# Kernel optimization log

Hardware: AMD Instinct MI355X
Metric: run time of the kernel (lower is better)

## Reference

```python
import jax, jax.numpy as jnp
import numpy as np
from jax import lax

B, C, H, W = 64, 3, 256, 256
E, D = 64, 32          # expert_nums, embed_dim
TOP_K = 2
NOISE_EPS = 0.01
ALPHA = 0.8


def setup_inputs() -> dict:
    key = jax.random.key(0)
    ks = jax.random.split(key, 16)
    n = lambda k, shape, s=0.05: jax.random.normal(k, shape, jnp.float32) * s
    return {
        "task_id": jax.random.randint(ks[0], (B,), 0, 10),
        "degradation_info": jax.random.normal(ks[1], (B, C, H, W), jnp.float32),
        "noise": jax.random.normal(ks[2], (B, E), jnp.float32),
        "mlp_w1": n(ks[3], (1, D)), "mlp_b1": jnp.zeros((D,), jnp.float32),
        "mlp_w2": n(ks[4], (D, D)), "mlp_b2": jnp.zeros((D,), jnp.float32),
        "conv1_w": n(ks[5], (16, C, 3, 3)), "conv1_b": jnp.zeros((16,), jnp.float32),
        "conv2_w": n(ks[6], (32, 16, 3, 3)), "conv2_b": jnp.zeros((32,), jnp.float32),
        "deg_w": n(ks[7], (32, D)), "deg_b": jnp.zeros((D,), jnp.float32),
        "expert_keys": jax.random.normal(ks[8], (E, D), jnp.float32),
        "gate_w": n(ks[9], (E, E)), "gate_b": jnp.zeros((E,), jnp.float32),
        "noise_w": n(ks[10], (E, E)), "noise_b": jnp.zeros((E,), jnp.float32),
    }


def _conv(x, w):
    return lax.conv_general_dilated(
        x, w, window_strides=(1, 1), padding="SAME",
        dimension_numbers=("NCHW", "OIHW", "NCHW"))


def reference(task_id, degradation_info, noise,
              mlp_w1, mlp_b1, mlp_w2, mlp_b2,
              conv1_w, conv1_b, conv2_w, conv2_b,
              deg_w, deg_b, expert_keys,
              gate_w, gate_b, noise_w, noise_b):
    # task embedding: Linear(1,D) -> ReLU -> Linear(D,D)
    t = task_id.astype(jnp.float32)[:, None]                       # [B,1]
    task_embed = jax.nn.relu(t @ mlp_w1 + mlp_b1) @ mlp_w2 + mlp_b2  # [B,D]

    # degradation conv embed: conv->relu->conv->relu->global avg pool
    h = jax.nn.relu(_conv(degradation_info, conv1_w) + conv1_b[None, :, None, None])
    h = jax.nn.relu(_conv(h, conv2_w) + conv2_b[None, :, None, None])
    feat = h.mean(axis=(2, 3))                                     # [B,32]
    deg_embed = feat @ deg_w + deg_b                               # [B,D]

    combined = task_embed + (1.0 - ALPHA) * deg_embed              # [B,D]
    sim = combined @ expert_keys.T / jnp.sqrt(jnp.float32(D))      # [B,E]
    expert_weight = jax.nn.softmax(sim, axis=1)

    clean_logits = expert_weight @ gate_w + gate_b                 # [B,E]
    stddev = jax.nn.softplus(expert_weight @ noise_w + noise_b) + NOISE_EPS
    logits = clean_logits + noise * stddev                         # train=True path

    top_logits, top_idx = lax.top_k(logits, min(TOP_K + 1, E))
    tk_logits = top_logits[:, :TOP_K]                              # [B,k]
    tk_idx = top_idx[:, :TOP_K]
    tk_gates = jax.nn.softmax(tk_logits, axis=1)

    rows = jnp.arange(logits.shape[0])[:, None]
    gates = jnp.zeros_like(logits).at[rows, tk_idx].set(tk_gates)  # scatter
    load = gates.sum(axis=0)                                       # [E]
    return gates, load
```

## Files before the change

### kernel.cpp

```cpp
#include <hip/hip_runtime.h>
#include <math.h>

typedef __attribute__((ext_vector_type(8)))  short  short8;
typedef __attribute__((ext_vector_type(4)))  short  svec4;
typedef __attribute__((ext_vector_type(4)))  float  floatx4;
typedef __attribute__((ext_vector_type(16))) float  floatx16;
typedef __attribute__((ext_vector_type(2)))  float  floatx2;
typedef __attribute__((ext_vector_type(2)))  unsigned uintx2;

__device__ __forceinline__ short bf16rne(float f) {
    unsigned u = __float_as_uint(f);
    unsigned r = (u + 0x7FFFu + ((u >> 16) & 1u)) >> 16;
    return (short)r;
}
__device__ __forceinline__ unsigned pk2(float a, float b) {
#if __has_builtin(__builtin_amdgcn_cvt_pk_bf16_f32)
    auto t = __builtin_amdgcn_cvt_pk_bf16_f32(a, b);
    unsigned u; __builtin_memcpy(&u, &t, 4); return u;
#else
    return (unsigned)(unsigned short)bf16rne(a) |
           ((unsigned)(unsigned short)bf16rne(b) << 16);
#endif
}
__device__ __forceinline__ floatx2 pkmax0(floatx2 a) {
#if __has_builtin(__builtin_elementwise_max)
    floatx2 z = {0.f, 0.f};
    return __builtin_elementwise_max(a, z);
#else
    floatx2 r; r.x = fmaxf(a.x, 0.f); r.y = fmaxf(a.y, 0.f); return r;
#endif
}

#define WS_FRAG_OFF  8192
#define WS_BIAS1_OFF (WS_FRAG_OFF + 11 * 64 * 16)
#define WS_BIAS2_OFF (WS_BIAS1_OFF + 64 * 16)

#define PLANE_B 18496

__global__ __launch_bounds__(256) void build_frags_kernel(
    const float* __restrict__ w1,
    const float* __restrict__ b1,
    const float* __restrict__ w2,
    const float* __restrict__ b2,
    void* __restrict__ ws,
    float* __restrict__ out)
{
    const int t = threadIdx.x;
    float* feat = (float*)ws;
    for (int i = t; i < 2048; i += 256) feat[i] = 0.0f;
    if (t >= 64 && t < 128) out[4096 + (t - 64)] = 0.0f;

    if (t < 64) {
        const int lane = t;
        const int q = lane >> 4, ml = lane & 15;
        const int n32 = lane & 31, half = lane >> 5;
        short8* F = (short8*)((char*)ws + WS_FRAG_OFF);

        short8 W1a;
#pragma unroll
        for (int j = 0; j < 8; ++j) {
            int p = q * 2 + (j >> 2), c = j & 3;
            W1a[j] = (c < 3) ? bf16rne(w1[ml * 27 + c * 9 + p]) : (short)0;
        }
        F[0 * 64 + lane] = W1a;

        short8 W1b;
#pragma unroll
        for (int j = 0; j < 8; ++j) {
            W1b[j] = (q == 0 && j < 3) ? bf16rne(w1[ml * 27 + j * 9 + 8])
                                       : (short)0;
        }
        F[1 * 64 + lane] = W1b;

#pragma unroll
        for (int s = 0; s < 9; ++s) {
            short8 Bs;
#pragma unroll
            for (int j = 0; j < 8; ++j) {
                int ic = half * 8 + j;
                Bs[j] = bf16rne(w2[(n32 * 16 + ic) * 9 + s]);
            }
            F[(2 + s) * 64 + lane] = Bs;
        }
        floatx4 bv;
#pragma unroll
        for (int r = 0; r < 4; ++r) bv[r] = b1[q * 4 + r];
        ((floatx4*)((char*)ws + WS_BIAS1_OFF))[lane] = bv;
        ((float*)((char*)ws + WS_BIAS2_OFF))[lane] = b2[n32];
    }
}

__device__ __forceinline__ void conv1_tile(
    char* __restrict__ wptr, const char* __restrict__ inb,
    const int* lcB, int gbyte, int wbyte, bool valid, bool wmask,
    short8 W1a, short8 W1b, floatx4 biasv)
{
    svec4 r0 = *(const svec4*)(inb + gbyte + lcB[0]);
    svec4 r1 = *(const svec4*)(inb + gbyte + lcB[1]);
    svec4 r2 = *(const svec4*)(inb + gbyte + lcB[2]);
    short8 Bx = __builtin_shufflevector(r0, r1, 0, 1, 2, 3, 4, 5, 6, 7);
    short8 By = __builtin_shufflevector(r2, r0, 0, 1, 2, 3, 4, 5, 6, 7);
    floatx4 acc = __builtin_amdgcn_mfma_f32_16x16x32_bf16(W1a, Bx, biasv,
                                                          0, 0, 0);
    acc = __builtin_amdgcn_mfma_f32_16x16x32_bf16(W1b, By, acc, 0, 0, 0);
    floatx2 lo = {acc[0], acc[1]}, hi = {acc[2], acc[3]};
    lo = pkmax0(lo); hi = pkmax0(hi);
    if (!valid) { floatx2 z = {0.f, 0.f}; lo = z; hi = z; }
    if (wmask) {
        uintx2 w; w.x = pk2(lo.x, lo.y); w.y = pk2(hi.x, hi.y);
        *(uintx2*)(wptr + wbyte) = w;
    }
}

__global__ __launch_bounds__(256, 3) void conv_feat_kernel(
    const float* __restrict__ x,
    const void*  __restrict__ ws_ro,
    float* __restrict__ feat_sum)
{
    __shared__ short s_in4[36 * 36 * 4];
    __shared__ short s_h1[2 * 9248];
    __shared__ float s_part[4][32];

    const int t    = threadIdx.x;
    const int lane = t & 63, wv = t >> 6;
    const int q    = lane >> 4, ml = lane & 15;
    const int n32  = lane & 31, half = lane >> 5;
    const int tx = blockIdx.x, ty = blockIdx.y, b = blockIdx.z;
    const bool border = (tx == 0) | (tx == 7) | (ty == 0) | (ty == 7);

    const short8* F = (const short8*)((const char*)ws_ro + WS_FRAG_OFF);
    short8 W1a = F[0 * 64 + lane];
    short8 W1b = F[1 * 64 + lane];
    short8 B2[9];
#pragma unroll
    for (int s = 0; s < 9; ++s) B2[s] = F[(2 + s) * 64 + lane];
    floatx4 biasv = ((const floatx4*)((const char*)ws_ro + WS_BIAS1_OFF))[lane];
    float   b2v   = ((const float*)((const char*)ws_ro + WS_BIAS2_OFF))[lane];

    int lcB[3];
    {
        int p0 = q * 2, p1 = q * 2 + 1;
        lcB[0] = ((p0 / 3) * 36 + p0 % 3) * 8;
        lcB[1] = ((p1 / 3) * 36 + p1 % 3) * 8;
        lcB[2] = (2 * 36 + 2) * 8;
    }

    const int gy0 = ty * 32 - 2, gx0 = tx * 32 - 2;
    const float* xb = x + (size_t)b * 3 * 65536;
    if (!border) {
        for (int i = t; i < 1296; i += 256) {
            int r = i / 36, c = i - r * 36;
            const float* p = xb + (gy0 + r) * 256 + gx0 + c;
            float v0 = p[0], v1 = p[65536], v2 = p[131072];
            uintx2 w; w.x = pk2(v0, v1); w.y = pk2(v2, 0.f);
            *(uintx2*)&s_in4[i * 4] = w;
        }
    } else {
        for (int i = t; i < 1296; i += 256) {
            int r = i / 36, c = i - r * 36;
            int gy = gy0 + r, gx = gx0 + c;
            float v0 = 0.f, v1 = 0.f, v2 = 0.f;
            if ((unsigned)gy < 256u && (unsigned)gx < 256u) {
                const float* p = xb + gy * 256 + gx;
                v0 = p[0]; v1 = p[65536]; v2 = p[131072];
            }
            uintx2 w; w.x = pk2(v0, v1); w.y = pk2(v2, 0.f);
            *(uintx2*)&s_in4[i * 4] = w;
        }
    }
    __syncthreads();

    char* wptr = (char*)s_h1 + (q >> 1) * PLANE_B + (q & 1) * 8;
    const char* inb = (const char*)s_in4;
    const int mlb = ml * 8, ml16 = ml * 16;
    if (!border) {
#pragma unroll
        for (int i = 0; i < 17; ++i) {
            int u = wv * 17 + i, row = u >> 1, ch = u & 1;
            conv1_tile(wptr, inb, lcB, row * 288 + ch * 128 + mlb,
                       row * 544 + ch * 256 + ml16, true, true,
                       W1a, W1b, biasv);
        }
        {
            int col = 32 + (wv >> 1), rb = (wv & 1) * 16;
            conv1_tile(wptr, inb, lcB, (rb + ml) * 288 + col * 8,
                       ml * 544 + (rb * 34 + col) * 16, true, true,
                       W1a, W1b, biasv);
        }
        if (wv == 0) {
            int ml2 = ml & 3;
            int iy = 32 + (ml2 >> 1), ix = 32 + (ml2 & 1);
            conv1_tile(wptr, inb, lcB, iy * 288 + ix * 8,
                       (iy * 34 + ix) * 16, true, ml < 4, W1a, W1b, biasv);
        }
    } else {
        const bool gxOK0 = (unsigned)(tx * 32 - 1 + ml) < 256u;
        const bool gxOK1 = (unsigned)(tx * 32 + 15 + ml) < 256u;
#pragma unroll
        for (int i = 0; i < 17; ++i) {
            int u = wv * 17 + i, row = u >> 1, ch = u & 1;
            bool ok = ((unsigned)(ty * 32 - 1 + row) < 256u) &
                      (ch ? gxOK1 : gxOK0);
            conv1_tile(wptr, inb, lcB, row * 288 + ch * 128 + mlb,
                       row * 544 + ch * 256 + ml16, ok, true,
                       W1a, W1b, biasv);
        }
        {
            int col = 32 + (wv >> 1), rb = (wv & 1) * 16;
            bool ok = ((unsigned)(ty * 32 - 1 + rb + ml) < 256u) &
                      ((unsigned)(tx * 32 - 1 + col) < 256u);
            conv1_tile(wptr, inb, lcB, (rb + ml) * 288 + col * 8,
                       ml * 544 + (rb * 34 + col) * 16, ok, true,
                       W1a, W1b, biasv);
        }
        if (wv == 0) {
            int ml2 = ml & 3;
            int iy = 32 + (ml2 >> 1), ix = 32 + (ml2 & 1);
            bool ok = ((unsigned)(ty * 32 - 1 + iy) < 256u) &
                      ((unsigned)(tx * 32 - 1 + ix) < 256u);
            conv1_tile(wptr, inb, lcB, iy * 288 + ix * 8,
                       (iy * 34 + ix) * 16, ok, ml < 4, W1a, W1b, biasv);
        }
    }
    __syncthreads();

    float part;
    {
        const int prow0 = n32 >> 4, pcol = n32 & 15;
        const int ch = wv >> 1, tp0 = (wv & 1) * 8;
        const int ox = ch * 16 + pcol;
        const char* pl = (const char*)s_h1 + half * PLANE_B;
        int pb = ((2 * tp0 + prow0) * 34 + ox) * 16;
        short8 Af[3][3];
#pragma unroll
        for (int ky = 0; ky < 3; ++ky)
#pragma unroll
            for (int kx = 0; kx < 3; ++kx)
                Af[ky][kx] = *(const short8*)(pl + pb + (ky * 34 + kx) * 16);

        floatx16 bias16;
#pragma unroll
        for (int r = 0; r < 16; ++r) bias16[r] = b2v;

        floatx2 p2 = {0.f, 0.f};
#pragma unroll
        for (int it = 0; it < 8; ++it) {
            const int rb = (2 * it) % 3;
            floatx16 acc = __builtin_amdgcn_mfma_f32_32x32x16_bf16(
                    Af[rb][0], B2[0], bias16, 0, 0, 0);
#pragma unroll
            for (int s = 1; s < 9; ++s) {
                const int ky = s / 3, kx = s % 3;
                acc = __builtin_amdgcn_mfma_f32_32x32x16_bf16(
                        Af[(rb + ky) % 3][kx], B2[s], acc, 0, 0, 0);
            }
#pragma unroll
            for (int r = 0; r < 16; r += 2) {
                floatx2 a2 = {acc[r], acc[r + 1]};
                p2 += pkmax0(a2);
            }
            if (it < 7) {
                pb += 1088;
#pragma unroll
                for (int kx = 0; kx < 3; ++kx) {
                    Af[rb][kx] =
                        *(const short8*)(pl + pb + (1 * 34 + kx) * 16);
                    Af[(rb + 1) % 3][kx] =
                        *(const short8*)(pl + pb + (2 * 34 + kx) * 16);
                }
            }
        }
        part = p2.x + p2.y;
    }
    part += __shfl_xor(part, 32);
    if (lane < 32) s_part[wv][n32] = part;
    __syncthreads();
    if (t < 32) {
        float ssum = s_part[0][t] + s_part[1][t] + s_part[2][t] + s_part[3][t];
        atomicAdd(feat_sum + b * 32 + t, ssum);
    }
}

__global__ __launch_bounds__(64) void router_gate_kernel(
    const int* __restrict__ task_id,
    const float* __restrict__ noise,
    const float* __restrict__ mlp_w1,
    const float* __restrict__ mlp_b1,
    const float* __restrict__ mlp_w2,
    const float* __restrict__ mlp_b2,
    const float* __restrict__ deg_w,
    const float* __restrict__ deg_b,
    const float* __restrict__ keys,
    const float* __restrict__ gate_w,
    const float* __restrict__ gate_b,
    const float* __restrict__ noise_w,
    const float* __restrict__ noise_b,
    const float* __restrict__ feat_sum,
    float* __restrict__ out)
{
    const int b = blockIdx.x;
    const int e = threadIdx.x;

    __shared__ float s_te[32];
    __shared__ float s_comb[32];
    __shared__ float s_ew[64];

    if (e < 32) {
        float tf = (float)task_id[b];
        s_te[e] = fmaxf(tf * mlp_w1[e] + mlp_b1[e], 0.0f);
    }
    __syncthreads();
    if (e < 32) {
        float acc = mlp_b2[e];
        for (int k = 0; k < 32; ++k) acc += s_te[k] * mlp_w2[k * 32 + e];
        float dacc = deg_b[e];
        for (int c = 0; c < 32; ++c)
            dacc += (feat_sum[b * 32 + c] * (1.0f / 65536.0f)) * deg_w[c * 32 + e];
        s_comb[e] = acc + 0.2f * dacc;
    }
    __syncthreads();

    float s = 0.0f;
    for (int d = 0; d < 32; ++d) s += s_comb[d] * keys[e * 32 + d];
    s *= 0.17677669529663687f;

    float m = s;
    for (int off = 32; off; off >>= 1) m = fmaxf(m, __shfl_xor(m, off));
    float p = expf(s - m);
    float sum = p;
    for (int off = 32; off; off >>= 1) sum += __shfl_xor(sum, off);
    float w = p / sum;
    s_ew[e] = w;
    __syncthreads();

    float cl = gate_b[e], nz = noise_b[e];
    for (int k = 0; k < 64; ++k) {
        float ewk = s_ew[k];
        cl += ewk * gate_w[k * 64 + e];
        nz += ewk * noise_w[k * 64 + e];
    }
    float sp = (nz > 20.0f) ? nz : log1pf(expf(nz));
    float logit = cl + noise[b * 64 + e] * (sp + 0.01f);

    float v0 = logit; int i0 = e;
    for (int off = 32; off; off >>= 1) {
        float ov = __shfl_xor(v0, off);
        int   oi = __shfl_xor(i0, off);
        if (ov > v0 || (ov == v0 && oi < i0)) { v0 = ov; i0 = oi; }
    }
    float v1 = (e == i0) ? -INFINITY : logit; int i1 = e;
    for (int off = 32; off; off >>= 1) {
        float ov = __shfl_xor(v1, off);
        int   oi = __shfl_xor(i1, off);
        if (ov > v1 || (ov == v1 && oi < i1)) { v1 = ov; i1 = oi; }
    }

    float e1 = expf(v1 - v0);
    float g0 = 1.0f / (1.0f + e1);
    float g1 = e1 / (1.0f + e1);

    float g = (e == i0) ? g0 : (e == i1) ? g1 : 0.0f;
    out[b * 64 + e] = g;
    if (g != 0.0f) atomicAdd(out + 64 * 64 + e, g);
}

extern "C" void kernel_launch(void* const* d_in, const int* in_sizes, int n_in,
                              void* d_out, int out_size, void* d_ws, size_t ws_size,
                              hipStream_t stream) {
    const int*   task_id = (const int*)d_in[0];
    const float* x       = (const float*)d_in[1];
    const float* noise   = (const float*)d_in[2];
    const float* mlp_w1  = (const float*)d_in[3];
    const float* mlp_b1  = (const float*)d_in[4];
    const float* mlp_w2  = (const float*)d_in[5];
    const float* mlp_b2  = (const float*)d_in[6];
    const float* conv1_w = (const float*)d_in[7];
    const float* conv1_b = (const float*)d_in[8];
    const float* conv2_w = (const float*)d_in[9];
    const float* conv2_b = (const float*)d_in[10];
    const float* deg_w   = (const float*)d_in[11];
    const float* deg_b   = (const float*)d_in[12];
    const float* keys    = (const float*)d_in[13];
    const float* gate_w  = (const float*)d_in[14];
    const float* gate_b  = (const float*)d_in[15];
    const float* noise_w = (const float*)d_in[16];
    const float* noise_b = (const float*)d_in[17];

    float* out  = (float*)d_out;
    float* feat = (float*)d_ws;

    build_frags_kernel<<<1, 256, 0, stream>>>(conv1_w, conv1_b, conv2_w,
                                              conv2_b, d_ws, out);
    dim3 gridA(8, 8, 64);
    conv_feat_kernel<<<gridA, 256, 0, stream>>>(x, d_ws, feat);
    router_gate_kernel<<<64, 64, 0, stream>>>(
        task_id, noise, mlp_w1, mlp_b1, mlp_w2, mlp_b2, deg_w, deg_b, keys,
        gate_w, gate_b, noise_w, noise_b, feat, out);
}
```

Before: 176.4 us.

## Process two images per block and prefetch the second input during conv2

Each conv block now handles batch images bz and bz+32, and the grid's z dimension is halved. The second image's input tile is loaded into registers while conv2 of the first image runs, then packed into shared memory before the second conv1 pass. The aim is to hide global-load latency behind MFMA work and to amortize weight-fragment and bias loads across two images. In exchange it adds live registers under a 3-blocks-per-CU launch bound, which risks spills or lower occupancy, and it halves the number of blocks.

```diff
diff --git a/kernel.cpp b/kernel.cpp
--- a/kernel.cpp
+++ b/kernel.cpp
@@ -125,7 +125,7 @@
     const int lane = t & 63, wv = t >> 6;
     const int q    = lane >> 4, ml = lane & 15;
     const int n32  = lane & 31, half = lane >> 5;
-    const int tx = blockIdx.x, ty = blockIdx.y, b = blockIdx.z;
+    const int tx = blockIdx.x, ty = blockIdx.y, bz = blockIdx.z;
     const bool border = (tx == 0) | (tx == 7) | (ty == 0) | (ty == 7);
 
     const short8* F = (const short8*)((const char*)ws_ro + WS_FRAG_OFF);
@@ -136,6 +136,9 @@
     for (int s = 0; s < 9; ++s) B2[s] = F[(2 + s) * 64 + lane];
     floatx4 biasv = ((const floatx4*)((const char*)ws_ro + WS_BIAS1_OFF))[lane];
     float   b2v   = ((const float*)((const char*)ws_ro + WS_BIAS2_OFF))[lane];
+    floatx16 bias16;
+#pragma unroll
+    for (int r = 0; r < 16; ++r) bias16[r] = b2v;
 
     int lcB[3];
     {
@@ -146,11 +149,112 @@
     }
 
     const int gy0 = ty * 32 - 2, gx0 = tx * 32 - 2;
-    const float* xb = x + (size_t)b * 3 * 65536;
+    const float* xb0 = x + (size_t)bz * 3 * 65536;
+    const float* xb1 = xb0 + (size_t)32 * 3 * 65536;
+    const bool gxOK0 = (unsigned)(tx * 32 - 1 + ml) < 256u;
+    const bool gxOK1 = (unsigned)(tx * 32 + 15 + ml) < 256u;
+
+    auto do_conv1 = [&]() {
+        char* wptr = (char*)s_h1 + (q >> 1) * PLANE_B + (q & 1) * 8;
+        const char* inb = (const char*)s_in4;
+        const int mlb = ml * 8, ml16 = ml * 16;
+        if (!border) {
+#pragma unroll
+            for (int i = 0; i < 17; ++i) {
+                int u = wv * 17 + i, row = u >> 1, ch = u & 1;
+                conv1_tile(wptr, inb, lcB, row * 288 + ch * 128 + mlb,
+                           row * 544 + ch * 256 + ml16, true, true,
+                           W1a, W1b, biasv);
+            }
+            {
+                int col = 32 + (wv >> 1), rb = (wv & 1) * 16;
+                conv1_tile(wptr, inb, lcB, (rb + ml) * 288 + col * 8,
+                           ml * 544 + (rb * 34 + col) * 16, true, true,
+                           W1a, W1b, biasv);
+            }
+            if (wv == 0) {
+                int ml2 = ml & 3;
+                int iy = 32 + (ml2 >> 1), ix = 32 + (ml2 & 1);
+                conv1_tile(wptr, inb, lcB, iy * 288 + ix * 8,
+                           (iy * 34 + ix) * 16, true, ml < 4, W1a, W1b, biasv);
+            }
+        } else {
+#pragma unroll
+            for (int i = 0; i < 17; ++i) {
+                int u = wv * 17 + i, row = u >> 1, ch = u & 1;
+                bool ok = ((unsigned)(ty * 32 - 1 + row) < 256u) &
+                          (ch ? gxOK1 : gxOK0);
+                conv1_tile(wptr, inb, lcB, row * 288 + ch * 128 + mlb,
+                           row * 544 + ch * 256 + ml16, ok, true,
+                           W1a, W1b, biasv);
+            }
+            {
+                int col = 32 + (wv >> 1), rb = (wv & 1) * 16;
+                bool ok = ((unsigned)(ty * 32 - 1 + rb + ml) < 256u) &
+                          ((unsigned)(tx * 32 - 1 + col) < 256u);
+                conv1_tile(wptr, inb, lcB, (rb + ml) * 288 + col * 8,
+                           ml * 544 + (rb * 34 + col) * 16, ok, true,
+                           W1a, W1b, biasv);
+            }
+            if (wv == 0) {
+                int ml2 = ml & 3;
+                int iy = 32 + (ml2 >> 1), ix = 32 + (ml2 & 1);
+                bool ok = ((unsigned)(ty * 32 - 1 + iy) < 256u) &
+                          ((unsigned)(tx * 32 - 1 + ix) < 256u);
+                conv1_tile(wptr, inb, lcB, iy * 288 + ix * 8,
+                           (iy * 34 + ix) * 16, ok, ml < 4, W1a, W1b, biasv);
+            }
+        }
+    };
+
+    auto do_conv2 = [&]() -> float {
+        const int prow0 = n32 >> 4, pcol = n32 & 15;
+        const int ch = wv >> 1, tp0 = (wv & 1) * 8;
+        const int ox = ch * 16 + pcol;
+        const char* pl = (const char*)s_h1 + half * PLANE_B;
+        int pb = ((2 * tp0 + prow0) * 34 + ox) * 16;
+        short8 Af[3][3];
+#pragma unroll
+        for (int ky = 0; ky < 3; ++ky)
+#pragma unroll
+            for (int kx = 0; kx < 3; ++kx)
+                Af[ky][kx] = *(const short8*)(pl + pb + (ky * 34 + kx) * 16);
+
+        floatx2 p2 = {0.f, 0.f};
+#pragma unroll
+        for (int it = 0; it < 8; ++it) {
+            const int rb = (2 * it) % 3;
+            floatx16 acc = __builtin_amdgcn_mfma_f32_32x32x16_bf16(
+                    Af[rb][0], B2[0], bias16, 0, 0, 0);
+#pragma unroll
+            for (int s = 1; s < 9; ++s) {
+                const int ky = s / 3, kx = s % 3;
+                acc = __builtin_amdgcn_mfma_f32_32x32x16_bf16(
+                        Af[(rb + ky) % 3][kx], B2[s], acc, 0, 0, 0);
+            }
+#pragma unroll
+            for (int r = 0; r < 16; r += 2) {
+                floatx2 a2 = {acc[r], acc[r + 1]};
+                p2 += pkmax0(a2);
+            }
+            if (it < 7) {
+                pb += 1088;
+#pragma unroll
+                for (int kx = 0; kx < 3; ++kx) {
+                    Af[rb][kx] =
+                        *(const short8*)(pl + pb + (1 * 34 + kx) * 16);
+                    Af[(rb + 1) % 3][kx] =
+                        *(const short8*)(pl + pb + (2 * 34 + kx) * 16);
+                }
+            }
+        }
+        return p2.x + p2.y;
+    };
+
     if (!border) {
         for (int i = t; i < 1296; i += 256) {
             int r = i / 36, c = i - r * 36;
-            const float* p = xb + (gy0 + r) * 256 + gx0 + c;
+            const float* p = xb0 + (gy0 + r) * 256 + gx0 + c;
             float v0 = p[0], v1 = p[65536], v2 = p[131072];
             uintx2 w; w.x = pk2(v0, v1); w.y = pk2(v2, 0.f);
             *(uintx2*)&s_in4[i * 4] = w;
@@ -161,7 +265,7 @@
             int gy = gy0 + r, gx = gx0 + c;
             float v0 = 0.f, v1 = 0.f, v2 = 0.f;
             if ((unsigned)gy < 256u && (unsigned)gx < 256u) {
-                const float* p = xb + gy * 256 + gx;
+                const float* p = xb0 + gy * 256 + gx;
                 v0 = p[0]; v1 = p[65536]; v2 = p[131072];
             }
             uintx2 w; w.x = pk2(v0, v1); w.y = pk2(v2, 0.f);
@@ -170,114 +274,66 @@
     }
     __syncthreads();
 
-    char* wptr = (char*)s_h1 + (q >> 1) * PLANE_B + (q & 1) * 8;
-    const char* inb = (const char*)s_in4;
-    const int mlb = ml * 8, ml16 = ml * 16;
+    do_conv1();
+    __syncthreads();
+
+    float sv0[6], sv1[6], sv2[6];
     if (!border) {
 #pragma unroll
-        for (int i = 0; i < 17; ++i) {
-            int u = wv * 17 + i, row = u >> 1, ch = u & 1;
-            conv1_tile(wptr, inb, lcB, row * 288 + ch * 128 + mlb,
-                       row * 544 + ch * 256 + ml16, true, true,
-                       W1a, W1b, biasv);
-        }
-        {
-            int col = 32 + (wv >> 1), rb = (wv & 1) * 16;
-            conv1_tile(wptr, inb, lcB, (rb + ml) * 288 + col * 8,
-                       ml * 544 + (rb * 34 + col) * 16, true, true,
-                       W1a, W1b, biasv);
-        }
-        if (wv == 0) {
-            int ml2 = ml & 3;
-            int iy = 32 + (ml2 >> 1), ix = 32 + (ml2 & 1);
-            conv1_tile(wptr, inb, lcB, iy * 288 + ix * 8,
-                       (iy * 34 + ix) * 16, true, ml < 4, W1a, W1b, biasv);
+        for (int it = 0; it < 6; ++it) {
+            int i = t + it * 256;
+            if (i < 1296) {
+                int r = i / 36, c = i - r * 36;
+                const float* p = xb1 + (gy0 + r) * 256 + gx0 + c;
+                sv0[it] = p[0]; sv1[it] = p[65536]; sv2[it] = p[131072];
+            }
         }
     } else {
-        const bool gxOK0 = (unsigned)(tx * 32 - 1 + ml) < 256u;
-        const bool gxOK1 = (unsigned)(tx * 32 + 15 + ml) < 256u;
-#pragma unroll
-        for (int i = 0; i < 17; ++i) {
-            int u = wv * 17 + i, row = u >> 1, ch = u & 1;
-            bool ok = ((unsigned)(ty * 32 - 1 + row) < 256u) &
-                      (ch ? gxOK1 : gxOK0);
-            conv1_tile(wptr, inb, lcB, row * 288 + ch * 128 + mlb,
-                       row * 544 + ch * 256 + ml16, ok, true,
-                       W1a, W1b, biasv);
-        }
-        {
-            int col = 32 + (wv >> 1), rb = (wv & 1) * 16;
-            bool ok = ((unsigned)(ty * 32 - 1 + rb + ml) < 256u) &
-                      ((unsigned)(tx * 32 - 1 + col) < 256u);
-            conv1_tile(wptr, inb, lcB, (rb + ml) * 288 + col * 8,
-                       ml * 544 + (rb * 34 + col) * 16, ok, true,
-                       W1a, W1b, biasv);
-        }
-        if (wv == 0) {
-            int ml2 = ml & 3;
-            int iy = 32 + (ml2 >> 1), ix = 32 + (ml2 & 1);
-            bool ok = ((unsigned)(ty * 32 - 1 + iy) < 256u) &
-                      ((unsigned)(tx * 32 - 1 + ix) < 256u);
-            conv1_tile(wptr, inb, lcB, iy * 288 + ix * 8,
-                       (iy * 34 + ix) * 16, ok, ml < 4, W1a, W1b, biasv);
-        }
-    }
-    __syncthreads();
-
-    float part;
-    {
-        const int prow0 = n32 >> 4, pcol = n32 & 15;
-        const int ch = wv >> 1, tp0 = (wv & 1) * 8;
-        const int ox = ch * 16 + pcol;
-        const char* pl = (const char*)s_h1 + half * PLANE_B;
-        int pb = ((2 * tp0 + prow0) * 34 + ox) * 16;
-        short8 Af[3][3];
-#pragma unroll
-        for (int ky = 0; ky < 3; ++ky)
-#pragma unroll
-            for (int kx = 0; kx < 3; ++kx)
-                Af[ky][kx] = *(const short8*)(pl + pb + (ky * 34 + kx) * 16);
-
-        floatx16 bias16;
-#pragma unroll
-        for (int r = 0; r < 16; ++r) bias16[r] = b2v;
-
-        floatx2 p2 = {0.f, 0.f};
-#pragma unroll
-        for (int it = 0; it < 8; ++it) {
-            const int rb = (2 * it) % 3;
-            floatx16 acc = __builtin_amdgcn_mfma_f32_32x32x16_bf16(
-                    Af[rb][0], B2[0], bias16, 0, 0, 0);
-#pragma unroll
-            for (int s = 1; s < 9; ++s) {
-                const int ky = s / 3, kx = s % 3;
-                acc = __builtin_amdgcn_mfma_f32_32x32x16_bf16(
-                        Af[(rb + ky) % 3][kx], B2[s], acc, 0, 0, 0);
-            }
-#pragma unroll
-            for (int r = 0; r < 16; r += 2) {
-                floatx2 a2 = {acc[r], acc[r + 1]};
-                p2 += pkmax0(a2);
-            }
-            if (it < 7) {
-                pb += 1088;
-#pragma unroll
-                for (int kx = 0; kx < 3; ++kx) {
-                    Af[rb][kx] =
-                        *(const short8*)(pl + pb + (1 * 34 + kx) * 16);
-                    Af[(rb + 1) % 3][kx] =
-                        *(const short8*)(pl + pb + (2 * 34 + kx) * 16);
+#pragma unroll
+        for (int it = 0; it < 6; ++it) {
+            int i = t + it * 256;
+            if (i < 1296) {
+                int r = i / 36, c = i - r * 36;
+                int gy = gy0 + r, gx = gx0 + c;
+                float a = 0.f, b = 0.f, cc = 0.f;
+                if ((unsigned)gy < 256u && (unsigned)gx < 256u) {
+                    const float* p = xb1 + gy * 256 + gx;
+                    a = p[0]; b = p[65536]; cc = p[131072];
                 }
-            }
-        }
-        part = p2.x + p2.y;
-    }
-    part += __shfl_xor(part, 32);
-    if (lane < 32) s_part[wv][n32] = part;
+                sv0[it] = a; sv1[it] = b; sv2[it] = cc;
+            }
+        }
+    }
+
+    float part0 = do_conv2();
+
+#pragma unroll
+    for (int it = 0; it < 6; ++it) {
+        int i = t + it * 256;
+        if (i < 1296) {
+            uintx2 w; w.x = pk2(sv0[it], sv1[it]); w.y = pk2(sv2[it], 0.f);
+            *(uintx2*)&s_in4[i * 4] = w;
+        }
+    }
+
+    part0 += __shfl_xor(part0, 32);
+    if (lane < 32) s_part[wv][n32] = part0;
     __syncthreads();
     if (t < 32) {
         float ssum = s_part[0][t] + s_part[1][t] + s_part[2][t] + s_part[3][t];
-        atomicAdd(feat_sum + b * 32 + t, ssum);
+        atomicAdd(feat_sum + bz * 32 + t, ssum);
+    }
+
+    do_conv1();
+    __syncthreads();
+
+    float part1 = do_conv2();
+    part1 += __shfl_xor(part1, 32);
+    if (lane < 32) s_part[wv][n32] = part1;
+    __syncthreads();
+    if (t < 32) {
+        float ssum = s_part[0][t] + s_part[1][t] + s_part[2][t] + s_part[3][t];
+        atomicAdd(feat_sum + (bz + 32) * 32 + t, ssum);
     }
 }
 
@@ -391,7 +447,7 @@
 
     build_frags_kernel<<<1, 256, 0, stream>>>(conv1_w, conv1_b, conv2_w,
                                               conv2_b, d_ws, out);
-    dim3 gridA(8, 8, 64);
+    dim3 gridA(8, 8, 32);
     conv_feat_kernel<<<gridA, 256, 0, stream>>>(x, d_ws, feat);
     router_gate_kernel<<<64, 64, 0, stream>>>(
         task_id, noise, mlp_w1, mlp_b1, mlp_w2, mlp_b2, deg_w, deg_b, keys,
```

Result: slower. 285.2 us (+61.7%).

## Split conv1/conv2 into two row chunks to halve h1 LDS and raise occupancy

Applied to the files above, without the earlier changes.

The conv1 intermediate tile is now produced and consumed in two 16-row halves, so the shared h1 buffer holds only an 18-row band instead of the full 34-row tile. This roughly halves LDS per block, and the launch bound moves from 3 to 5 blocks per CU to hide latency better. In exchange each block needs two extra barriers, and conv1 recomputes the two overlapping halo rows between chunks.

```diff
diff --git a/kernel.cpp b/kernel.cpp
--- a/kernel.cpp
+++ b/kernel.cpp
@@ -35,7 +35,7 @@
 #define WS_BIAS1_OFF (WS_FRAG_OFF + 11 * 64 * 16)
 #define WS_BIAS2_OFF (WS_BIAS1_OFF + 64 * 16)
 
-#define PLANE_B 18496
+#define PLANE_B 9792
 
 __global__ __launch_bounds__(256) void build_frags_kernel(
     const float* __restrict__ w1,
@@ -112,13 +112,116 @@
     }
 }
 
-__global__ __launch_bounds__(256, 3) void conv_feat_kernel(
+__device__ __forceinline__ void conv1_chunk(
+    int r0, bool border, int tx, int ty, int wv, int q, int ml,
+    const int* lcB, char* __restrict__ s_h1, const char* __restrict__ inb,
+    short8 W1a, short8 W1b, floatx4 biasv)
+{
+    char* wptr = s_h1 + (q >> 1) * PLANE_B + (q & 1) * 8;
+    const int mlb = ml * 8, ml16 = ml * 16;
+    const int gbase = r0 * 288;
+    if (!border) {
+#pragma unroll
+        for (int i = 0; i < 9; ++i) {
+            int u = wv * 9 + i, row = u >> 1, ch = u & 1;
+            conv1_tile(wptr, inb, lcB, gbase + row * 288 + ch * 128 + mlb,
+                       row * 544 + ch * 256 + ml16, true, true,
+                       W1a, W1b, biasv);
+        }
+        if (wv < 2) {
+            int col = 32 + wv;
+            conv1_tile(wptr, inb, lcB, gbase + ml * 288 + col * 8,
+                       ml * 544 + col * 16, true, true, W1a, W1b, biasv);
+        }
+        if (wv == 2) {
+            int ml2 = ml & 3;
+            int iy = 16 + (ml2 >> 1), ix = 32 + (ml2 & 1);
+            conv1_tile(wptr, inb, lcB, gbase + iy * 288 + ix * 8,
+                       (iy * 34 + ix) * 16, true, ml < 4, W1a, W1b, biasv);
+        }
+    } else {
+        const int gyb = ty * 32 - 1 + r0;
+        const bool gxOK0 = (unsigned)(tx * 32 - 1 + ml) < 256u;
+        const bool gxOK1 = (unsigned)(tx * 32 + 15 + ml) < 256u;
+#pragma unroll
+        for (int i = 0; i < 9; ++i) {
+            int u = wv * 9 + i, row = u >> 1, ch = u & 1;
+            bool ok = ((unsigned)(gyb + row) < 256u) & (ch ? gxOK1 : gxOK0);
+            conv1_tile(wptr, inb, lcB, gbase + row * 288 + ch * 128 + mlb,
+                       row * 544 + ch * 256 + ml16, ok, true,
+                       W1a, W1b, biasv);
+        }
+        if (wv < 2) {
+            int col = 32 + wv;
+            bool ok = ((unsigned)(gyb + ml) < 256u) &
+                      ((unsigned)(tx * 32 - 1 + col) < 256u);
+            conv1_tile(wptr, inb, lcB, gbase + ml * 288 + col * 8,
+                       ml * 544 + col * 16, ok, true, W1a, W1b, biasv);
+        }
+        if (wv == 2) {
+            int ml2 = ml & 3;
+            int iy = 16 + (ml2 >> 1), ix = 32 + (ml2 & 1);
+            bool ok = ((unsigned)(gyb + iy) < 256u) &
+                      ((unsigned)(tx * 32 - 1 + ix) < 256u);
+            conv1_tile(wptr, inb, lcB, gbase + iy * 288 + ix * 8,
+                       (iy * 34 + ix) * 16, ok, ml < 4, W1a, W1b, biasv);
+        }
+    }
+}
+
+__device__ __forceinline__ float conv2_chunk(
+    int wv, int n32, int half, const char* __restrict__ s_h1,
+    const short8* __restrict__ B2, floatx16 bias16)
+{
+    const int prow0 = n32 >> 4, pcol = n32 & 15;
+    const int ch = wv >> 1, rbase = (wv & 1) * 8;
+    const int ox = ch * 16 + pcol;
+    const char* pl = s_h1 + half * PLANE_B;
+    int pb = ((rbase + prow0) * 34 + ox) * 16;
+    short8 Af[3][3];
+#pragma unroll
+    for (int ky = 0; ky < 3; ++ky)
+#pragma unroll
+        for (int kx = 0; kx < 3; ++kx)
+            Af[ky][kx] = *(const short8*)(pl + pb + (ky * 34 + kx) * 16);
+
+    floatx2 p2 = {0.f, 0.f};
+#pragma unroll
+    for (int it = 0; it < 4; ++it) {
+        const int rb = (2 * it) % 3;
+        floatx16 acc = __builtin_amdgcn_mfma_f32_32x32x16_bf16(
+                Af[rb][0], B2[0], bias16, 0, 0, 0);
+#pragma unroll
+        for (int s = 1; s < 9; ++s) {
+            const int ky = s / 3, kx = s % 3;
+            acc = __builtin_amdgcn_mfma_f32_32x32x16_bf16(
+                    Af[(rb + ky) % 3][kx], B2[s], acc, 0, 0, 0);
+        }
+#pragma unroll
+        for (int r = 0; r < 16; r += 2) {
+            floatx2 a2 = {acc[r], acc[r + 1]};
+            p2 += pkmax0(a2);
+        }
+        if (it < 3) {
+            pb += 1088;
+#pragma unroll
+            for (int kx = 0; kx < 3; ++kx) {
+                Af[rb][kx] = *(const short8*)(pl + pb + (1 * 34 + kx) * 16);
+                Af[(rb + 1) % 3][kx] =
+                    *(const short8*)(pl + pb + (2 * 34 + kx) * 16);
+            }
+        }
+    }
+    return p2.x + p2.y;
+}
+
+__global__ __launch_bounds__(256, 5) void conv_feat_kernel(
     const float* __restrict__ x,
     const void*  __restrict__ ws_ro,
     float* __restrict__ feat_sum)
 {
     __shared__ short s_in4[36 * 36 * 4];
-    __shared__ short s_h1[2 * 9248];
+    __shared__ short s_h1[2 * 4896];
     __shared__ float s_part[4][32];
 
     const int t    = threadIdx.x;
@@ -136,6 +239,9 @@
     for (int s = 0; s < 9; ++s) B2[s] = F[(2 + s) * 64 + lane];
     floatx4 biasv = ((const floatx4*)((const char*)ws_ro + WS_BIAS1_OFF))[lane];
     float   b2v   = ((const float*)((const char*)ws_ro + WS_BIAS2_OFF))[lane];
+    floatx16 bias16;
+#pragma unroll
+    for (int r = 0; r < 16; ++r) bias16[r] = b2v;
 
     int lcB[3];
     {
@@ -170,108 +276,17 @@
     }
     __syncthreads();
 
-    char* wptr = (char*)s_h1 + (q >> 1) * PLANE_B + (q & 1) * 8;
-    const char* inb = (const char*)s_in4;
-    const int mlb = ml * 8, ml16 = ml * 16;
-    if (!border) {
-#pragma unroll
-        for (int i = 0; i < 17; ++i) {
-            int u = wv * 17 + i, row = u >> 1, ch = u & 1;
-            conv1_tile(wptr, inb, lcB, row * 288 + ch * 128 + mlb,
-                       row * 544 + ch * 256 + ml16, true, true,
-                       W1a, W1b, biasv);
-        }
-        {
-            int col = 32 + (wv >> 1), rb = (wv & 1) * 16;
-            conv1_tile(wptr, inb, lcB, (rb + ml) * 288 + col * 8,
-                       ml * 544 + (rb * 34 + col) * 16, true, true,
-                       W1a, W1b, biasv);
-        }
-        if (wv == 0) {
-            int ml2 = ml & 3;
-            int iy = 32 + (ml2 >> 1), ix = 32 + (ml2 & 1);
-            conv1_tile(wptr, inb, lcB, iy * 288 + ix * 8,
-                       (iy * 34 + ix) * 16, true, ml < 4, W1a, W1b, biasv);
-        }
-    } else {
-        const bool gxOK0 = (unsigned)(tx * 32 - 1 + ml) < 256u;
-        const bool gxOK1 = (unsigned)(tx * 32 + 15 + ml) < 256u;
-#pragma unroll
-        for (int i = 0; i < 17; ++i) {
-            int u = wv * 17 + i, row = u >> 1, ch = u & 1;
-            bool ok = ((unsigned)(ty * 32 - 1 + row) < 256u) &
-                      (ch ? gxOK1 : gxOK0);
-            conv1_tile(wptr, inb, lcB, row * 288 + ch * 128 + mlb,
-                       row * 544 + ch * 256 + ml16, ok, true,
-                       W1a, W1b, biasv);
-        }
-        {
-            int col = 32 + (wv >> 1), rb = (wv & 1) * 16;
-            bool ok = ((unsigned)(ty * 32 - 1 + rb + ml) < 256u) &
-                      ((unsigned)(tx * 32 - 1 + col) < 256u);
-            conv1_tile(wptr, inb, lcB, (rb + ml) * 288 + col * 8,
-                       ml * 544 + (rb * 34 + col) * 16, ok, true,
-                       W1a, W1b, biasv);
-        }
-        if (wv == 0) {
-            int ml2 = ml & 3;
-            int iy = 32 + (ml2 >> 1), ix = 32 + (ml2 & 1);
-            bool ok = ((unsigned)(ty * 32 - 1 + iy) < 256u) &
-                      ((unsigned)(tx * 32 - 1 + ix) < 256u);
-            conv1_tile(wptr, inb, lcB, iy * 288 + ix * 8,
-                       (iy * 34 + ix) * 16, ok, ml < 4, W1a, W1b, biasv);
-        }
-    }
-    __syncthreads();
-
-    float part;
-    {
-        const int prow0 = n32 >> 4, pcol = n32 & 15;
-        const int ch = wv >> 1, tp0 = (wv & 1) * 8;
-        const int ox = ch * 16 + pcol;
-        const char* pl = (const char*)s_h1 + half * PLANE_B;
-        int pb = ((2 * tp0 + prow0) * 34 + ox) * 16;
-        short8 Af[3][3];
-#pragma unroll
-        for (int ky = 0; ky < 3; ++ky)
-#pragma unroll
-            for (int kx = 0; kx < 3; ++kx)
-                Af[ky][kx] = *(const short8*)(pl + pb + (ky * 34 + kx) * 16);
-
-        floatx16 bias16;
-#pragma unroll
-        for (int r = 0; r < 16; ++r) bias16[r] = b2v;
-
-        floatx2 p2 = {0.f, 0.f};
-#pragma unroll
-        for (int it = 0; it < 8; ++it) {
-            const int rb = (2 * it) % 3;
-            floatx16 acc = __builtin_amdgcn_mfma_f32_32x32x16_bf16(
-                    Af[rb][0], B2[0], bias16, 0, 0, 0);
-#pragma unroll
-            for (int s = 1; s < 9; ++s) {
-                const int ky = s / 3, kx = s % 3;
-                acc = __builtin_amdgcn_mfma_f32_32x32x16_bf16(
-                        Af[(rb + ky) % 3][kx], B2[s], acc, 0, 0, 0);
-            }
-#pragma unroll
-            for (int r = 0; r < 16; r += 2) {
-                floatx2 a2 = {acc[r], acc[r + 1]};
-                p2 += pkmax0(a2);
-            }
-            if (it < 7) {
-                pb += 1088;
-#pragma unroll
-                for (int kx = 0; kx < 3; ++kx) {
-                    Af[rb][kx] =
-                        *(const short8*)(pl + pb + (1 * 34 + kx) * 16);
-                    Af[(rb + 1) % 3][kx] =
-                        *(const short8*)(pl + pb + (2 * 34 + kx) * 16);
-                }
-            }
-        }
-        part = p2.x + p2.y;
-    }
+    conv1_chunk(0, border, tx, ty, wv, q, ml, lcB, (char*)s_h1,
+                (const char*)s_in4, W1a, W1b, biasv);
+    __syncthreads();
+    float part = conv2_chunk(wv, n32, half, (const char*)s_h1, B2, bias16);
+    __syncthreads();
+
+    conv1_chunk(16, border, tx, ty, wv, q, ml, lcB, (char*)s_h1,
+                (const char*)s_in4, W1a, W1b, biasv);
+    __syncthreads();
+    part += conv2_chunk(wv, n32, half, (const char*)s_h1, B2, bias16);
+
     part += __shfl_xor(part, 32);
     if (lane < 32) s_part[wv][n32] = part;
     __syncthreads();
```

Result: slower. 483.0 us (+173.9%).
